# Performance work log

Hardware: AMD Instinct MI355X
Metric: run time of the kernel (lower is better)

The kernel has to match this reference:

```python
import jax, jax.numpy as jnp
import numpy as np

B, S, DMODEL, HEADS = 2, 2048, 1024, 16
DK = DMODEL // HEADS
DV = DMODEL // HEADS


def setup_inputs() -> dict:
    key = jax.random.key(0)
    kx, kq, kk, kv = jax.random.split(key, 4)
    x = jax.random.normal(kx, (B, S, DMODEL), dtype=jnp.float32)
    # stacked per-head projection weights, shape [H, dmodel, dk/dv]
    # (equivalent to nn.Linear(dmodel, dk, bias=False) per head)
    scale = 1.0 / np.sqrt(DMODEL)
    Wq = jax.random.uniform(kq, (HEADS, DMODEL, DK), jnp.float32, -scale, scale)
    Wk = jax.random.uniform(kk, (HEADS, DMODEL, DK), jnp.float32, -scale, scale)
    Wv = jax.random.uniform(kv, (HEADS, DMODEL, DV), jnp.float32, -scale, scale)
    return {"x": x, "Wq": Wq, "Wk": Wk, "Wv": Wv}


def reference(x, Wq, Wk, Wv):
    # per-head projections, batched across heads: [B,H,S,dk]
    q = jnp.einsum("bsd,hdk->bhsk", x, Wq)
    k = jnp.einsum("bsd,hdk->bhsk", x, Wk)
    v = jnp.einsum("bsd,hdv->bhsv", x, Wv)
    # NOTE: original module applies NO 1/sqrt(dk) scaling — keep faithful
    scores = jnp.einsum("bhqk,bhsk->bhqs", q, k)  # [B,H,S,S]
    attn = jax.nn.softmax(scores, axis=-1)
    out = jnp.einsum("bhqs,bhsv->bhqv", attn, v)  # [B,H,S,dv]
    # concat heads along last dim in head order
    Bsz, H, Sq, Dv = out.shape
    return jnp.transpose(out, (0, 2, 1, 3)).reshape(Bsz, Sq, H * Dv)
```

## Files before the change

kernel.cpp:

```cpp
#include <hip/hip_runtime.h>

#define B_ 2
#define S_ 2048
#define D_ 1024
#define H_ 16
#define DK_ 64
#define M_ (B_ * S_)
#define N_ (3 * D_)

typedef __bf16 bf16x8 __attribute__((ext_vector_type(8)));
typedef short s8vec __attribute__((ext_vector_type(8)));
typedef float f4vec __attribute__((ext_vector_type(4)));

static __device__ __forceinline__ ushort f2b(float f) {
  union { float f; unsigned u; } v; v.f = f;
  unsigned u = v.u;
  u += 0x7FFFu + ((u >> 16) & 1u);
  return (ushort)(u >> 16);
}

static __device__ __forceinline__ unsigned pk2(float a, float b) {
#if __has_builtin(__builtin_amdgcn_cvt_pk_bf16_f32)
  typedef __bf16 b2 __attribute__((ext_vector_type(2)));
  b2 r = __builtin_amdgcn_cvt_pk_bf16_f32(a, b);
  return __builtin_bit_cast(unsigned, r);
#else
  return (unsigned)f2b(a) | ((unsigned)f2b(b) << 16);
#endif
}

static __device__ __forceinline__ f4vec mfma16(s8vec a, s8vec b, f4vec c) {
  return __builtin_amdgcn_mfma_f32_16x16x32_bf16(
      __builtin_bit_cast(bf16x8, a), __builtin_bit_cast(bf16x8, b), c, 0, 0, 0);
}

static __device__ __forceinline__ void gl_lds16(const ushort* g, ushort* l) {
  __builtin_amdgcn_global_load_lds(
      (const __attribute__((address_space(1))) unsigned*)g,
      (__attribute__((address_space(3))) unsigned*)l, 16, 0, 0);
}

static __device__ __forceinline__ void wg_barrier_lds() {
  asm volatile("" ::: "memory");
  __builtin_amdgcn_s_waitcnt(0xC07F);
  __builtin_amdgcn_s_barrier();
  asm volatile("" ::: "memory");
}

__global__ void cvt_x(const float* __restrict__ x, ushort* __restrict__ xb) {
  int i = blockIdx.x * 256 + threadIdx.x;
  float4 v = ((const float4*)x)[i];
  ushort4 o;
  o.x = f2b(v.x); o.y = f2b(v.y); o.z = f2b(v.z); o.w = f2b(v.w);
  ((ushort4*)xb)[i] = o;
}

__global__ __launch_bounds__(256) void cvt_w(const float* __restrict__ Wq,
                                             const float* __restrict__ Wk,
                                             const float* __restrict__ Wv,
                                             ushort* __restrict__ wbt) {
  __shared__ ushort T[64 * 72];
  const int w = blockIdx.z, h = blockIdx.y, d0 = blockIdx.x * 64;
  const float* W = (w == 0) ? Wq : (w == 1) ? Wk : Wv;
  const float* src = W + (size_t)h * 65536 + (size_t)d0 * 64;
  const int t = threadIdx.x;
#pragma unroll
  for (int j = 0; j < 4; ++j) {
    int idx = j * 256 + t;
    int dr = idx >> 4, kc = (idx & 15) * 4;
    float4 v = *(const float4*)(src + dr * 64 + kc);
    T[(kc + 0) * 72 + dr] = f2b(v.x);
    T[(kc + 1) * 72 + dr] = f2b(v.y);
    T[(kc + 2) * 72 + dr] = f2b(v.z);
    T[(kc + 3) * 72 + dr] = f2b(v.w);
  }
  __syncthreads();
  const int kk = t >> 2, dcg = (t & 3) * 16;
  ushort* dst = wbt + ((size_t)w * 1024 + h * 64 + kk) * 1024 + d0 + dcg;
  *(s8vec*)dst       = *(const s8vec*)&T[kk * 72 + dcg];
  *(s8vec*)(dst + 8) = *(const s8vec*)&T[kk * 72 + dcg + 8];
}

__global__ __launch_bounds__(256) void proj_gemm(const ushort* __restrict__ xb,
                                                 const ushort* __restrict__ wbt,
                                                 ushort* __restrict__ qkv) {
  __shared__ __attribute__((aligned(16))) ushort As[128 * 64];
  __shared__ __attribute__((aligned(16))) ushort Bs[128 * 64];
  const int tid = threadIdx.x, wid = tid >> 6, lane = tid & 63;
  const int quad = lane >> 4, l15 = lane & 15;
  const int wm = wid & 1, wn = wid >> 1;
  const int m0 = blockIdx.x * 128, n0 = blockIdx.y * 128;

  f4vec acc[4][4];
#pragma unroll
  for (int mb = 0; mb < 4; mb++)
#pragma unroll
    for (int nb = 0; nb < 4; nb++)
#pragma unroll
      for (int i = 0; i < 4; i++) acc[mb][nb][i] = 0.f;

  const int sr = tid >> 3, sg = tid & 7;
  const int lg = sg ^ (sr & 7);
  const ushort* Ab = xb + (size_t)m0 * D_;
  const ushort* Bb = wbt + (size_t)n0 * D_;

  for (int k0 = 0; k0 < D_; k0 += 64) {
    __syncthreads();
#pragma unroll
    for (int j = 0; j < 4; ++j) {
      int r = j * 32 + sr;
      gl_lds16(Ab + (size_t)r * D_ + k0 + lg * 8, &As[j * 2048 + wid * 512]);
      gl_lds16(Bb + (size_t)r * D_ + k0 + lg * 8, &Bs[j * 2048 + wid * 512]);
    }
    __syncthreads();

#pragma unroll
    for (int kb = 0; kb < 2; ++kb) {
      s8vec af[4], bf[4];
#pragma unroll
      for (int mb = 0; mb < 4; ++mb) {
        int m = wm * 64 + mb * 16 + l15;
        int gpos = (kb * 4 + quad) ^ (m & 7);
        af[mb] = *(const s8vec*)&As[m * 64 + gpos * 8];
      }
#pragma unroll
      for (int nb = 0; nb < 4; ++nb) {
        int n = wn * 64 + nb * 16 + l15;
        int gpos = (kb * 4 + quad) ^ (n & 7);
        bf[nb] = *(const s8vec*)&Bs[n * 64 + gpos * 8];
      }
#pragma unroll
      for (int mb = 0; mb < 4; ++mb)
#pragma unroll
        for (int nb = 0; nb < 4; ++nb)
          acc[mb][nb] = mfma16(af[mb], bf[nb], acc[mb][nb]);
    }
  }

  const size_t per = (size_t)B_ * H_ * S_ * DK_;
  const int w = n0 >> 10;
  if (w == 2) {
    ushort* vt = qkv + 2 * per;
#pragma unroll
    for (int mb = 0; mb < 4; ++mb)
#pragma unroll
      for (int nb = 0; nb < 4; ++nb)
#pragma unroll
        for (int i = 0; i < 4; ++i) {
          int m = m0 + wm * 64 + mb * 16 + quad * 4 + i;
          int b = m >> 11, s = m & 2047;
          int n1 = (n0 & 1023) + wn * 64 + nb * 16 + l15;
          vt[((size_t)b * 1024 + n1) * S_ + s] = f2b(acc[mb][nb][i]);
        }
  } else {
#pragma unroll
    for (int mb = 0; mb < 4; ++mb)
#pragma unroll
      for (int nb = 0; nb < 4; ++nb)
#pragma unroll
        for (int i = 0; i < 4; ++i) {
          int m = m0 + wm * 64 + mb * 16 + quad * 4 + i;
          int b = m >> 11, s = m & 2047;
          int n1 = (n0 & 1023) + wn * 64 + nb * 16 + l15;
          qkv[(size_t)w * per + (((size_t)b * H_ + (n1 >> 6)) * S_ + s) * 64 + (n1 & 63)] =
              f2b(acc[mb][nb][i]);
        }
  }
}

__global__ __launch_bounds__(512) void attn(const ushort* __restrict__ qg,
                                            const ushort* __restrict__ kg,
                                            const ushort* __restrict__ vtg,
                                            float* __restrict__ out) {
  __shared__ __attribute__((aligned(16))) ushort Ks[128 * 64];
  __shared__ __attribute__((aligned(16))) ushort Vt[2][64 * 64];
  __shared__ __attribute__((aligned(16))) ushort Ps[8][16 * 132];
  const int qt = blockIdx.x, bh = blockIdx.y;
  const int b = bh >> 4, h = bh & 15;
  const int tid = threadIdx.x, wid = tid >> 6, lane = tid & 63;
  const int quad = lane >> 4, l15 = lane & 15, l7 = l15 & 7;

  const ushort* qbase = qg + ((size_t)bh * S_ + qt * 128 + wid * 16) * DK_;
  s8vec aq0 = *(const s8vec*)(qbase + (size_t)l15 * DK_ + quad * 8);
  s8vec aq1 = *(const s8vec*)(qbase + (size_t)l15 * DK_ + 32 + quad * 8);

  f4vec o[4];
  float lsum[4];
#pragma unroll
  for (int i = 0; i < 4; i++) {
    lsum[i] = 0.f;
#pragma unroll
    for (int nb = 0; nb < 4; nb++) o[nb][i] = 0.f;
  }

  const int r = tid >> 3, gs = tid & 7;
  const int gk = gs ^ (r & 7);
  const ushort* kb_ = kg + (size_t)bh * S_ * DK_;
  const ushort* vb_ = vtg + (size_t)bh * 64 * S_ + (size_t)r * S_;

  s8vec kr0 = *(const s8vec*)(kb_ + (size_t)r * DK_ + gk * 8);
  s8vec kr1 = *(const s8vec*)(kb_ + (size_t)(64 + r) * DK_ + gk * 8);
  s8vec vr0 = *(const s8vec*)(vb_ + gk * 8);
  s8vec vr1 = *(const s8vec*)(vb_ + 64 + gk * 8);

  for (int kt = 0; kt < S_ / 128; ++kt) {
    wg_barrier_lds();
    *(s8vec*)&Ks[r * 64 + gs * 8]        = kr0;
    *(s8vec*)&Ks[(64 + r) * 64 + gs * 8] = kr1;
    *(s8vec*)&Vt[0][r * 64 + gs * 8]     = vr0;
    *(s8vec*)&Vt[1][r * 64 + gs * 8]     = vr1;
    if (kt + 1 < S_ / 128) {
      const ushort* kn = kb_ + (size_t)((kt + 1) * 128 + r) * DK_ + gk * 8;
      kr0 = *(const s8vec*)(kn);
      kr1 = *(const s8vec*)(kn + (size_t)64 * DK_);
      const ushort* vn = vb_ + (kt + 1) * 128 + gk * 8;
      vr0 = *(const s8vec*)(vn);
      vr1 = *(const s8vec*)(vn + 64);
    }
    wg_barrier_lds();

    f4vec sc[8];
#pragma unroll
    for (int nb = 0; nb < 8; nb++) {
#pragma unroll
      for (int i = 0; i < 4; i++) sc[nb][i] = 0.f;
      const int row = nb * 16 + l15;
      s8vec bk0 = *(const s8vec*)&Ks[row * 64 + ((0 + quad) ^ l7) * 8];
      s8vec bk1 = *(const s8vec*)&Ks[row * 64 + ((4 + quad) ^ l7) * 8];
      sc[nb] = mfma16(aq0, bk0, sc[nb]);
      sc[nb] = mfma16(aq1, bk1, sc[nb]);
    }

#pragma unroll
    for (int nb = 0; nb < 8; nb++) {
#pragma unroll
      for (int i = 0; i < 4; i++) {
        float p = __expf(sc[nb][i]);
        sc[nb][i] = p;
        lsum[i] += p;
      }
      unsigned p01 = pk2(sc[nb][0], sc[nb][1]);
      unsigned p23 = pk2(sc[nb][2], sc[nb][3]);
      ushort* pw = &Ps[wid][quad * 4 * 132 + nb * 16 + l15];
      pw[0]   = (ushort)p01;
      pw[132] = (ushort)(p01 >> 16);
      pw[264] = (ushort)p23;
      pw[396] = (ushort)(p23 >> 16);
    }

#pragma unroll
    for (int kb2 = 0; kb2 < 4; kb2++) {
      s8vec ap = *(const s8vec*)(&Ps[wid][l15 * 132 + kb2 * 32 + quad * 8]);
      const int half = kb2 >> 1, G = (kb2 & 1) * 4 + quad;
#pragma unroll
      for (int nb = 0; nb < 4; nb++) {
        s8vec bv = *(const s8vec*)&Vt[half][(nb * 16 + l15) * 64 + (G ^ l7) * 8];
        o[nb] = mfma16(ap, bv, o[nb]);
      }
    }
  }

#pragma unroll
  for (int i = 0; i < 4; i++) {
#pragma unroll
    for (int msk = 1; msk < 16; msk <<= 1) lsum[i] += __shfl_xor(lsum[i], msk, 64);
  }

  float* ob = out + ((size_t)b * S_ + qt * 128 + wid * 16) * D_ + h * DK_;
#pragma unroll
  for (int i = 0; i < 4; i++) {
    float inv = 1.0f / lsum[i];
#pragma unroll
    for (int nb = 0; nb < 4; nb++)
      ob[(size_t)(quad * 4 + i) * D_ + nb * 16 + l15] = o[nb][i] * inv;
  }
}

extern "C" void kernel_launch(void* const* d_in, const int* in_sizes, int n_in,
                              void* d_out, int out_size, void* d_ws, size_t ws_size,
                              hipStream_t stream) {
  const float* x  = (const float*)d_in[0];
  const float* Wq = (const float*)d_in[1];
  const float* Wk = (const float*)d_in[2];
  const float* Wv = (const float*)d_in[3];
  float* out = (float*)d_out;

  ushort* xb  = (ushort*)d_ws;
  ushort* wbt = xb + (size_t)B_ * S_ * D_;
  ushort* qkv = wbt + (size_t)3 * D_ * D_;
  const size_t per = (size_t)B_ * H_ * S_ * DK_;

  cvt_x<<<(B_ * S_ * D_) / 4 / 256, 256, 0, stream>>>(x, xb);
  cvt_w<<<dim3(16, 16, 3), 256, 0, stream>>>(Wq, Wk, Wv, wbt);
  proj_gemm<<<dim3(M_ / 128, N_ / 128), 256, 0, stream>>>(xb, wbt, qkv);
  attn<<<dim3(S_ / 128, B_ * H_), 512, 0, stream>>>(qkv, qkv + per, qkv + 2 * per, out);
}
```

Baseline: 175.2 us.

## Give each attention wave 32 query rows and fold log2e into Q for exp2

The attention kernel moves from 8 waves of 16 query rows to 4 waves of 32 rows each, so every K and V fragment read from LDS feeds two MFMAs instead of one. The projection GEMM now scales Q by log2(e) before the bf16 store, which lets the softmax use the hardware exp2 instruction in place of expf. The intent is to cut LDS traffic per MFMA and the cost of the exponential. The trade-off is more registers per wave, fewer waves per block, and slightly different rounding of the pre-scaled Q.

Result: no change. 176.9 us (+0.9%).

```diff
diff --git a/kernel.cpp b/kernel.cpp
--- a/kernel.cpp
+++ b/kernel.cpp
@@ -26,6 +26,14 @@
   return __builtin_bit_cast(unsigned, r);
 #else
   return (unsigned)f2b(a) | ((unsigned)f2b(b) << 16);
+#endif
+}
+
+static __device__ __forceinline__ float fexp2(float x) {
+#if __has_builtin(__builtin_amdgcn_exp2f)
+  return __builtin_amdgcn_exp2f(x);
+#else
+  return exp2f(x);
 #endif
 }
 
@@ -153,6 +161,7 @@
           vt[((size_t)b * 1024 + n1) * S_ + s] = f2b(acc[mb][nb][i]);
         }
   } else {
+    const float qs = (w == 0) ? 1.44269504f : 1.0f;
 #pragma unroll
     for (int mb = 0; mb < 4; ++mb)
 #pragma unroll
@@ -163,116 +172,146 @@
           int b = m >> 11, s = m & 2047;
           int n1 = (n0 & 1023) + wn * 64 + nb * 16 + l15;
           qkv[(size_t)w * per + (((size_t)b * H_ + (n1 >> 6)) * S_ + s) * 64 + (n1 & 63)] =
-              f2b(acc[mb][nb][i]);
+              f2b(acc[mb][nb][i] * qs);
         }
   }
 }
 
-__global__ __launch_bounds__(512) void attn(const ushort* __restrict__ qg,
+__global__ __launch_bounds__(256) void attn(const ushort* __restrict__ qg,
                                             const ushort* __restrict__ kg,
                                             const ushort* __restrict__ vtg,
                                             float* __restrict__ out) {
   __shared__ __attribute__((aligned(16))) ushort Ks[128 * 64];
   __shared__ __attribute__((aligned(16))) ushort Vt[2][64 * 64];
-  __shared__ __attribute__((aligned(16))) ushort Ps[8][16 * 132];
+  __shared__ __attribute__((aligned(16))) ushort Ps[4][32 * 132];
   const int qt = blockIdx.x, bh = blockIdx.y;
   const int b = bh >> 4, h = bh & 15;
   const int tid = threadIdx.x, wid = tid >> 6, lane = tid & 63;
   const int quad = lane >> 4, l15 = lane & 15, l7 = l15 & 7;
 
-  const ushort* qbase = qg + ((size_t)bh * S_ + qt * 128 + wid * 16) * DK_;
-  s8vec aq0 = *(const s8vec*)(qbase + (size_t)l15 * DK_ + quad * 8);
-  s8vec aq1 = *(const s8vec*)(qbase + (size_t)l15 * DK_ + 32 + quad * 8);
-
-  f4vec o[4];
-  float lsum[4];
-#pragma unroll
-  for (int i = 0; i < 4; i++) {
-    lsum[i] = 0.f;
-#pragma unroll
-    for (int nb = 0; nb < 4; nb++) o[nb][i] = 0.f;
-  }
+  const ushort* qbase = qg + ((size_t)bh * S_ + qt * 128 + wid * 32) * DK_;
+  s8vec aq[2][2];
+#pragma unroll
+  for (int mb = 0; mb < 2; mb++) {
+    aq[mb][0] = *(const s8vec*)(qbase + (size_t)(mb * 16 + l15) * DK_ + quad * 8);
+    aq[mb][1] = *(const s8vec*)(qbase + (size_t)(mb * 16 + l15) * DK_ + 32 + quad * 8);
+  }
+
+  f4vec o[2][4];
+  float lsum[2][4];
+#pragma unroll
+  for (int mb = 0; mb < 2; mb++)
+#pragma unroll
+    for (int i = 0; i < 4; i++) {
+      lsum[mb][i] = 0.f;
+#pragma unroll
+      for (int nb = 0; nb < 4; nb++) o[mb][nb][i] = 0.f;
+    }
 
   const int r = tid >> 3, gs = tid & 7;
   const int gk = gs ^ (r & 7);
   const ushort* kb_ = kg + (size_t)bh * S_ * DK_;
-  const ushort* vb_ = vtg + (size_t)bh * 64 * S_ + (size_t)r * S_;
-
-  s8vec kr0 = *(const s8vec*)(kb_ + (size_t)r * DK_ + gk * 8);
-  s8vec kr1 = *(const s8vec*)(kb_ + (size_t)(64 + r) * DK_ + gk * 8);
-  s8vec vr0 = *(const s8vec*)(vb_ + gk * 8);
-  s8vec vr1 = *(const s8vec*)(vb_ + 64 + gk * 8);
+  const ushort* vb_ = vtg + (size_t)bh * 64 * S_;
+
+  s8vec kpre[4], vpre[4];
+#pragma unroll
+  for (int j = 0; j < 4; ++j)
+    kpre[j] = *(const s8vec*)(kb_ + (size_t)(j * 32 + r) * DK_ + gk * 8);
+  vpre[0] = *(const s8vec*)(vb_ + (size_t)r * S_ + gk * 8);
+  vpre[1] = *(const s8vec*)(vb_ + (size_t)r * S_ + 64 + gk * 8);
+  vpre[2] = *(const s8vec*)(vb_ + (size_t)(r + 32) * S_ + gk * 8);
+  vpre[3] = *(const s8vec*)(vb_ + (size_t)(r + 32) * S_ + 64 + gk * 8);
 
   for (int kt = 0; kt < S_ / 128; ++kt) {
     wg_barrier_lds();
-    *(s8vec*)&Ks[r * 64 + gs * 8]        = kr0;
-    *(s8vec*)&Ks[(64 + r) * 64 + gs * 8] = kr1;
-    *(s8vec*)&Vt[0][r * 64 + gs * 8]     = vr0;
-    *(s8vec*)&Vt[1][r * 64 + gs * 8]     = vr1;
+#pragma unroll
+    for (int j = 0; j < 4; ++j)
+      *(s8vec*)&Ks[(j * 32 + r) * 64 + gs * 8] = kpre[j];
+    *(s8vec*)&Vt[0][r * 64 + gs * 8]        = vpre[0];
+    *(s8vec*)&Vt[1][r * 64 + gs * 8]        = vpre[1];
+    *(s8vec*)&Vt[0][(r + 32) * 64 + gs * 8] = vpre[2];
+    *(s8vec*)&Vt[1][(r + 32) * 64 + gs * 8] = vpre[3];
     if (kt + 1 < S_ / 128) {
       const ushort* kn = kb_ + (size_t)((kt + 1) * 128 + r) * DK_ + gk * 8;
-      kr0 = *(const s8vec*)(kn);
-      kr1 = *(const s8vec*)(kn + (size_t)64 * DK_);
-      const ushort* vn = vb_ + (kt + 1) * 128 + gk * 8;
-      vr0 = *(const s8vec*)(vn);
-      vr1 = *(const s8vec*)(vn + 64);
+#pragma unroll
+      for (int j = 0; j < 4; ++j)
+        kpre[j] = *(const s8vec*)(kn + (size_t)(j * 32) * DK_);
+      const ushort* vn = vb_ + (size_t)r * S_ + (kt + 1) * 128 + gk * 8;
+      vpre[0] = *(const s8vec*)(vn);
+      vpre[1] = *(const s8vec*)(vn + 64);
+      vpre[2] = *(const s8vec*)(vn + (size_t)32 * S_);
+      vpre[3] = *(const s8vec*)(vn + (size_t)32 * S_ + 64);
     }
     wg_barrier_lds();
 
-    f4vec sc[8];
+    f4vec sc[2][8];
 #pragma unroll
     for (int nb = 0; nb < 8; nb++) {
-#pragma unroll
-      for (int i = 0; i < 4; i++) sc[nb][i] = 0.f;
       const int row = nb * 16 + l15;
       s8vec bk0 = *(const s8vec*)&Ks[row * 64 + ((0 + quad) ^ l7) * 8];
       s8vec bk1 = *(const s8vec*)&Ks[row * 64 + ((4 + quad) ^ l7) * 8];
-      sc[nb] = mfma16(aq0, bk0, sc[nb]);
-      sc[nb] = mfma16(aq1, bk1, sc[nb]);
-    }
-
-#pragma unroll
-    for (int nb = 0; nb < 8; nb++) {
-#pragma unroll
-      for (int i = 0; i < 4; i++) {
-        float p = __expf(sc[nb][i]);
-        sc[nb][i] = p;
-        lsum[i] += p;
-      }
-      unsigned p01 = pk2(sc[nb][0], sc[nb][1]);
-      unsigned p23 = pk2(sc[nb][2], sc[nb][3]);
-      ushort* pw = &Ps[wid][quad * 4 * 132 + nb * 16 + l15];
-      pw[0]   = (ushort)p01;
-      pw[132] = (ushort)(p01 >> 16);
-      pw[264] = (ushort)p23;
-      pw[396] = (ushort)(p23 >> 16);
-    }
+#pragma unroll
+      for (int mb = 0; mb < 2; mb++) {
+        f4vec z;
+#pragma unroll
+        for (int i = 0; i < 4; i++) z[i] = 0.f;
+        z = mfma16(aq[mb][0], bk0, z);
+        sc[mb][nb] = mfma16(aq[mb][1], bk1, z);
+      }
+    }
+
+#pragma unroll
+    for (int mb = 0; mb < 2; mb++)
+#pragma unroll
+      for (int nb = 0; nb < 8; nb++) {
+#pragma unroll
+        for (int i = 0; i < 4; i++) {
+          float p = fexp2(sc[mb][nb][i]);
+          sc[mb][nb][i] = p;
+          lsum[mb][i] += p;
+        }
+        unsigned p01 = pk2(sc[mb][nb][0], sc[mb][nb][1]);
+        unsigned p23 = pk2(sc[mb][nb][2], sc[mb][nb][3]);
+        ushort* pw = &Ps[wid][(mb * 16 + quad * 4) * 132 + nb * 16 + l15];
+        pw[0]   = (ushort)p01;
+        pw[132] = (ushort)(p01 >> 16);
+        pw[264] = (ushort)p23;
+        pw[396] = (ushort)(p23 >> 16);
+      }
 
 #pragma unroll
     for (int kb2 = 0; kb2 < 4; kb2++) {
-      s8vec ap = *(const s8vec*)(&Ps[wid][l15 * 132 + kb2 * 32 + quad * 8]);
+      s8vec ap0 = *(const s8vec*)(&Ps[wid][(l15) * 132 + kb2 * 32 + quad * 8]);
+      s8vec ap1 = *(const s8vec*)(&Ps[wid][(16 + l15) * 132 + kb2 * 32 + quad * 8]);
       const int half = kb2 >> 1, G = (kb2 & 1) * 4 + quad;
 #pragma unroll
       for (int nb = 0; nb < 4; nb++) {
         s8vec bv = *(const s8vec*)&Vt[half][(nb * 16 + l15) * 64 + (G ^ l7) * 8];
-        o[nb] = mfma16(ap, bv, o[nb]);
-      }
-    }
-  }
-
-#pragma unroll
-  for (int i = 0; i < 4; i++) {
-#pragma unroll
-    for (int msk = 1; msk < 16; msk <<= 1) lsum[i] += __shfl_xor(lsum[i], msk, 64);
-  }
-
-  float* ob = out + ((size_t)b * S_ + qt * 128 + wid * 16) * D_ + h * DK_;
-#pragma unroll
-  for (int i = 0; i < 4; i++) {
-    float inv = 1.0f / lsum[i];
-#pragma unroll
-    for (int nb = 0; nb < 4; nb++)
-      ob[(size_t)(quad * 4 + i) * D_ + nb * 16 + l15] = o[nb][i] * inv;
+        o[0][nb] = mfma16(ap0, bv, o[0][nb]);
+        o[1][nb] = mfma16(ap1, bv, o[1][nb]);
+      }
+    }
+  }
+
+#pragma unroll
+  for (int mb = 0; mb < 2; mb++)
+#pragma unroll
+    for (int i = 0; i < 4; i++) {
+#pragma unroll
+      for (int msk = 1; msk < 16; msk <<= 1)
+        lsum[mb][i] += __shfl_xor(lsum[mb][i], msk, 64);
+    }
+
+#pragma unroll
+  for (int mb = 0; mb < 2; mb++) {
+    float* ob = out + ((size_t)b * S_ + qt * 128 + wid * 32 + mb * 16) * D_ + h * DK_;
+#pragma unroll
+    for (int i = 0; i < 4; i++) {
+      float inv = 1.0f / lsum[mb][i];
+#pragma unroll
+      for (int nb = 0; nb < 4; nb++)
+        ob[(size_t)(quad * 4 + i) * D_ + nb * 16 + l15] = o[mb][nb][i] * inv;
+    }
   }
 }
 
@@ -293,5 +332,5 @@
   cvt_x<<<(B_ * S_ * D_) / 4 / 256, 256, 0, stream>>>(x, xb);
   cvt_w<<<dim3(16, 16, 3), 256, 0, stream>>>(Wq, Wk, Wv, wbt);
   proj_gemm<<<dim3(M_ / 128, N_ / 128), 256, 0, stream>>>(xb, wbt, qkv);
-  attn<<<dim3(S_ / 128, B_ * H_), 512, 0, stream>>>(qkv, qkv + per, qkv + 2 * per, out);
-}
+  attn<<<dim3(S_ / 128, B_ * H_), 256, 0, stream>>>(qkv, qkv + per, qkv + 2 * per, out);
+}
```
